# Optimization experiments

Hardware: AMD Instinct MI355X
Metric: run time of the kernel (lower is better)

Reference implementation:

```python
import jax, jax.numpy as jnp
import numpy as np

NUM_NODES = 100000
HIDDEN = 128
NUM_PATH = 8
PATH_LEN = 8


def setup_inputs() -> dict:
    key = jax.random.key(0)
    k1, k2, k3, k4, k5 = jax.random.split(key, 5)
    feats = jax.random.normal(k1, (NUM_NODES, HIDDEN), dtype=jnp.float32)
    paths = jax.random.randint(k2, (NUM_PATH, NUM_NODES, PATH_LEN), 0, NUM_NODES, dtype=jnp.int32)
    init_feats = jax.random.normal(k3, (NUM_NODES, HIDDEN), dtype=jnp.float32)
    # xavier_normal_ with gain=1.414 on (1, L, D): std = gain*sqrt(2/(fan_in+fan_out))
    pw_std = 1.414 * np.sqrt(2.0 / (PATH_LEN + HIDDEN))
    path_weight = pw_std * jax.random.normal(k4, (1, PATH_LEN, HIDDEN), dtype=jnp.float32)
    fc_std = 1.414 * np.sqrt(2.0 / (HIDDEN + HIDDEN))
    fc_w = fc_std * jax.random.normal(k5, (HIDDEN, HIDDEN), dtype=jnp.float32)
    return {"feats": feats, "paths": paths, "init_feats": init_feats,
            "path_weight": path_weight, "fc_w": fc_w}


def reference(feats, paths, init_feats, path_weight, fc_w):
    # feats: (N, D); paths: (P, N, L); path_weight: (1, L, D); fc_w: (D, D)
    w = path_weight[0]  # (L, D)

    def step(acc, path):
        g = feats[path]                      # (N, L, D) irregular gather
        acc = acc + jnp.einsum('nld,ld->nd', g, w)
        return acc, None

    acc, _ = jax.lax.scan(step, jnp.zeros_like(feats), paths)
    res = acc / paths.shape[0]               # mean over paths, (N, D)
    out = jax.nn.relu(res @ fc_w.T)          # Linear (no bias) + ReLU
    return out
```

## Files before the change

kernel.cpp:

```cpp
#include <hip/hip_runtime.h>
#include <hip/hip_fp16.h>


#define N_NODES 100000
#define HIDDEN  128
#define NPATH   8
#define PLEN    8
#define NPB     8
#define KT      32

__global__ void PathGCNLayer_61306363183203_tohalf(
    const float4* __restrict__ feats4,
    uint2*        __restrict__ fh)
{
    const size_t i = (size_t)blockIdx.x * blockDim.x + threadIdx.x;
    if (i < (size_t)N_NODES * 32) {
        const float4 v = feats4[i];
        __half2 a = __floats2half2_rn(v.x, v.y);
        __half2 b = __floats2half2_rn(v.z, v.w);
        uint2 o;
        o.x = *reinterpret_cast<unsigned int*>(&a);
        o.y = *reinterpret_cast<unsigned int*>(&b);
        fh[i] = o;
    }
}

__global__ void PathGCNLayer_61306363183203_fused_h(
    const uint2*  __restrict__ feats_h,
    const int*    __restrict__ paths,
    const float4* __restrict__ pw4,
    const float4* __restrict__ fcw4,
    float*        __restrict__ out)
{
    __shared__ int    sidx[NPATH * NPB * PLEN];
    __shared__ float4 sres4[NPB][33];
    __shared__ float  fcwt[HIDDEN][KT + 1];

    const int tid  = threadIdx.x;
    const int n0   = blockIdx.x * NPB;
    const int node = tid >> 5;
    const int c    = tid & 31;

    {
        const int p = tid >> 5;
        const int i = tid & 31;
        const size_t base = (size_t)p * (N_NODES * PLEN) + (size_t)n0 * PLEN;
        sidx[p * 64 + i]      = paths[base + i];
        sidx[p * 64 + i + 32] = paths[base + i + 32];
    }
    __syncthreads();

    float ax = 0.0f, ay = 0.0f, az = 0.0f, aw = 0.0f;
    #pragma unroll
    for (int l = 0; l < PLEN; ++l) {
        float sx = 0.0f, sy = 0.0f, sz = 0.0f, sw = 0.0f;
        #pragma unroll
        for (int p = 0; p < NPATH; ++p) {
            const int idx = sidx[p * 64 + node * PLEN + l];
            const uint2 hv = feats_h[(size_t)idx * 32 + c];
            const __half2 h0 = *reinterpret_cast<const __half2*>(&hv.x);
            const __half2 h1 = *reinterpret_cast<const __half2*>(&hv.y);
            const float2 f0 = __half22float2(h0);
            const float2 f1 = __half22float2(h1);
            sx += f0.x; sy += f0.y; sz += f1.x; sw += f1.y;
        }
        const float4 w = pw4[l * 32 + c];
        ax = fmaf(sx, w.x, ax);
        ay = fmaf(sy, w.y, ay);
        az = fmaf(sz, w.z, az);
        aw = fmaf(sw, w.w, aw);
    }
    {
        float4 r;
        r.x = ax * 0.125f; r.y = ay * 0.125f;
        r.z = az * 0.125f; r.w = aw * 0.125f;
        sres4[node][c] = r;
    }

    float o0 = 0.0f, o1 = 0.0f, o2 = 0.0f, o3 = 0.0f;

    #pragma unroll
    for (int kt = 0; kt < HIDDEN / KT; ++kt) {
        __syncthreads();
        {
            const int j    = tid >> 1;
            const int half = tid & 1;
            const int gbase = j * 32 + kt * (KT / 4) + half * 4;
            const int lbase = half * 16;
            #pragma unroll
            for (int q = 0; q < 4; ++q) {
                const float4 v = fcw4[gbase + q];
                fcwt[j][lbase + q * 4 + 0] = v.x;
                fcwt[j][lbase + q * 4 + 1] = v.y;
                fcwt[j][lbase + q * 4 + 2] = v.z;
                fcwt[j][lbase + q * 4 + 3] = v.w;
            }
        }
        __syncthreads();

        #pragma unroll
        for (int kc = 0; kc < KT / 4; ++kc) {
            const float4 rv = sres4[node][kt * (KT / 4) + kc];
            const int k0 = kc * 4;
            o0 = fmaf(rv.x, fcwt[c      ][k0    ], o0);
            o1 = fmaf(rv.x, fcwt[c + 32 ][k0    ], o1);
            o2 = fmaf(rv.x, fcwt[c + 64 ][k0    ], o2);
            o3 = fmaf(rv.x, fcwt[c + 96 ][k0    ], o3);
            o0 = fmaf(rv.y, fcwt[c      ][k0 + 1], o0);
            o1 = fmaf(rv.y, fcwt[c + 32 ][k0 + 1], o1);
            o2 = fmaf(rv.y, fcwt[c + 64 ][k0 + 1], o2);
            o3 = fmaf(rv.y, fcwt[c + 96 ][k0 + 1], o3);
            o0 = fmaf(rv.z, fcwt[c      ][k0 + 2], o0);
            o1 = fmaf(rv.z, fcwt[c + 32 ][k0 + 2], o1);
            o2 = fmaf(rv.z, fcwt[c + 64 ][k0 + 2], o2);
            o3 = fmaf(rv.z, fcwt[c + 96 ][k0 + 2], o3);
            o0 = fmaf(rv.w, fcwt[c      ][k0 + 3], o0);
            o1 = fmaf(rv.w, fcwt[c + 32 ][k0 + 3], o1);
            o2 = fmaf(rv.w, fcwt[c + 64 ][k0 + 3], o2);
            o3 = fmaf(rv.w, fcwt[c + 96 ][k0 + 3], o3);
        }
    }

    {
        const size_t obase = (size_t)(n0 + node) * HIDDEN + c;
        out[obase]      = o0 > 0.0f ? o0 : 0.0f;
        out[obase + 32] = o1 > 0.0f ? o1 : 0.0f;
        out[obase + 64] = o2 > 0.0f ? o2 : 0.0f;
        out[obase + 96] = o3 > 0.0f ? o3 : 0.0f;
    }
}

__global__ void PathGCNLayer_61306363183203_fused(
    const float4* __restrict__ feats4,
    const int*    __restrict__ paths,
    const float4* __restrict__ pw4,
    const float4* __restrict__ fcw4,
    float*        __restrict__ out)
{
    __shared__ int    sidx[NPATH * NPB * PLEN];
    __shared__ float4 sres4[NPB][33];
    __shared__ float  fcwt[HIDDEN][KT + 1];

    const int tid  = threadIdx.x;
    const int n0   = blockIdx.x * NPB;
    const int node = tid >> 5;
    const int c    = tid & 31;

    {
        const int p = tid >> 5;
        const int i = tid & 31;
        const size_t base = (size_t)p * (N_NODES * PLEN) + (size_t)n0 * PLEN;
        sidx[p * 64 + i]      = paths[base + i];
        sidx[p * 64 + i + 32] = paths[base + i + 32];
    }
    __syncthreads();

    float ax = 0.0f, ay = 0.0f, az = 0.0f, aw = 0.0f;
    #pragma unroll
    for (int l = 0; l < PLEN; ++l) {
        float sx = 0.0f, sy = 0.0f, sz = 0.0f, sw = 0.0f;
        #pragma unroll
        for (int p = 0; p < NPATH; ++p) {
            const int idx = sidx[p * 64 + node * PLEN + l];
            const float4 v = feats4[(size_t)idx * 32 + c];
            sx += v.x; sy += v.y; sz += v.z; sw += v.w;
        }
        const float4 w = pw4[l * 32 + c];
        ax = fmaf(sx, w.x, ax);
        ay = fmaf(sy, w.y, ay);
        az = fmaf(sz, w.z, az);
        aw = fmaf(sw, w.w, aw);
    }
    {
        float4 r;
        r.x = ax * 0.125f; r.y = ay * 0.125f;
        r.z = az * 0.125f; r.w = aw * 0.125f;
        sres4[node][c] = r;
    }

    float o0 = 0.0f, o1 = 0.0f, o2 = 0.0f, o3 = 0.0f;
    #pragma unroll
    for (int kt = 0; kt < HIDDEN / KT; ++kt) {
        __syncthreads();
        {
            const int j    = tid >> 1;
            const int half = tid & 1;
            const int gbase = j * 32 + kt * (KT / 4) + half * 4;
            const int lbase = half * 16;
            #pragma unroll
            for (int q = 0; q < 4; ++q) {
                const float4 v = fcw4[gbase + q];
                fcwt[j][lbase + q * 4 + 0] = v.x;
                fcwt[j][lbase + q * 4 + 1] = v.y;
                fcwt[j][lbase + q * 4 + 2] = v.z;
                fcwt[j][lbase + q * 4 + 3] = v.w;
            }
        }
        __syncthreads();
        #pragma unroll
        for (int kc = 0; kc < KT / 4; ++kc) {
            const float4 rv = sres4[node][kt * (KT / 4) + kc];
            const int k0 = kc * 4;
            o0 = fmaf(rv.x, fcwt[c      ][k0    ], o0);
            o1 = fmaf(rv.x, fcwt[c + 32 ][k0    ], o1);
            o2 = fmaf(rv.x, fcwt[c + 64 ][k0    ], o2);
            o3 = fmaf(rv.x, fcwt[c + 96 ][k0    ], o3);
            o0 = fmaf(rv.y, fcwt[c      ][k0 + 1], o0);
            o1 = fmaf(rv.y, fcwt[c + 32 ][k0 + 1], o1);
            o2 = fmaf(rv.y, fcwt[c + 64 ][k0 + 1], o2);
            o3 = fmaf(rv.y, fcwt[c + 96 ][k0 + 1], o3);
            o0 = fmaf(rv.z, fcwt[c      ][k0 + 2], o0);
            o1 = fmaf(rv.z, fcwt[c + 32 ][k0 + 2], o1);
            o2 = fmaf(rv.z, fcwt[c + 64 ][k0 + 2], o2);
            o3 = fmaf(rv.z, fcwt[c + 96 ][k0 + 2], o3);
            o0 = fmaf(rv.w, fcwt[c      ][k0 + 3], o0);
            o1 = fmaf(rv.w, fcwt[c + 32 ][k0 + 3], o1);
            o2 = fmaf(rv.w, fcwt[c + 64 ][k0 + 3], o2);
            o3 = fmaf(rv.w, fcwt[c + 96 ][k0 + 3], o3);
        }
    }
    {
        const size_t obase = (size_t)(n0 + node) * HIDDEN + c;
        out[obase]      = o0 > 0.0f ? o0 : 0.0f;
        out[obase + 32] = o1 > 0.0f ? o1 : 0.0f;
        out[obase + 64] = o2 > 0.0f ? o2 : 0.0f;
        out[obase + 96] = o3 > 0.0f ? o3 : 0.0f;
    }
}

extern "C" void kernel_launch(void* const* d_in, const int* in_sizes, int n_in,
                              void* d_out, int out_size, void* d_ws, size_t ws_size,
                              hipStream_t stream) {
    const float4* feats4 = (const float4*)d_in[0];
    const int*    paths  = (const int*)d_in[1];
    const float4* pw4    = (const float4*)d_in[3];
    const float4* fcw4   = (const float4*)d_in[4];
    float* out = (float*)d_out;
    (void)in_sizes; (void)n_in; (void)out_size;

    const size_t half_bytes = (size_t)N_NODES * HIDDEN * sizeof(unsigned short);
    if (d_ws != nullptr && ws_size >= half_bytes) {
        uint2* fh = (uint2*)d_ws;
        const int cvt_blocks = (N_NODES * 32 + 255) / 256;
        PathGCNLayer_61306363183203_tohalf<<<cvt_blocks, 256, 0, stream>>>(feats4, fh);
        PathGCNLayer_61306363183203_fused_h<<<N_NODES / NPB, 256, 0, stream>>>(
            fh, paths, pw4, fcw4, out);
    } else {
        PathGCNLayer_61306363183203_fused<<<N_NODES / NPB, 256, 0, stream>>>(
            feats4, paths, pw4, fcw4, out);
    }
}
```

Before: 367.5 us.

## Process 16 nodes per block with 16-byte half gathers and 8 outputs per thread

The half-precision fused kernel now handles 16 nodes per 256-thread block, with 16 threads per node. Each thread gathers a uint4 (8 halves) per neighbour instead of a uint2, and all 8 path loads are issued before accumulating. Each thread also computes 8 output columns in the FC stage, so the transposed weight tile is loaded once for twice as many nodes. The aim is wider memory transactions, more loads in flight and less redundant weight staging, at the cost of higher register use per thread.

```diff
diff --git a/kernel.cpp b/kernel.cpp
--- a/kernel.cpp
+++ b/kernel.cpp
@@ -6,7 +6,7 @@
 #define HIDDEN  128
 #define NPATH   8
 #define PLEN    8
-#define NPB     8
+#define NPB     16
 #define KT      32
 
 __global__ void PathGCNLayer_61306363183203_tohalf(
@@ -25,8 +25,8 @@
     }
 }
 
-__global__ void PathGCNLayer_61306363183203_fused_h(
-    const uint2*  __restrict__ feats_h,
+__global__ void PathGCNLayer_61306363183203_fused_h16(
+    const uint4*  __restrict__ feats_h4,
     const int*    __restrict__ paths,
     const float4* __restrict__ pw4,
     const float4* __restrict__ fcw4,
@@ -38,46 +38,78 @@
 
     const int tid  = threadIdx.x;
     const int n0   = blockIdx.x * NPB;
-    const int node = tid >> 5;
-    const int c    = tid & 31;
+    const int node = tid >> 4;
+    const int c    = tid & 15;
 
     {
         const int p = tid >> 5;
         const int i = tid & 31;
         const size_t base = (size_t)p * (N_NODES * PLEN) + (size_t)n0 * PLEN;
-        sidx[p * 64 + i]      = paths[base + i];
-        sidx[p * 64 + i + 32] = paths[base + i + 32];
+        sidx[p * 128 + i]      = paths[base + i];
+        sidx[p * 128 + i + 32] = paths[base + i + 32];
+        sidx[p * 128 + i + 64] = paths[base + i + 64];
+        sidx[p * 128 + i + 96] = paths[base + i + 96];
     }
     __syncthreads();
 
-    float ax = 0.0f, ay = 0.0f, az = 0.0f, aw = 0.0f;
+    float a0 = 0.f, a1 = 0.f, a2 = 0.f, a3 = 0.f,
+          a4 = 0.f, a5 = 0.f, a6 = 0.f, a7 = 0.f;
     #pragma unroll
     for (int l = 0; l < PLEN; ++l) {
-        float sx = 0.0f, sy = 0.0f, sz = 0.0f, sw = 0.0f;
-        #pragma unroll
-        for (int p = 0; p < NPATH; ++p) {
-            const int idx = sidx[p * 64 + node * PLEN + l];
-            const uint2 hv = feats_h[(size_t)idx * 32 + c];
-            const __half2 h0 = *reinterpret_cast<const __half2*>(&hv.x);
-            const __half2 h1 = *reinterpret_cast<const __half2*>(&hv.y);
-            const float2 f0 = __half22float2(h0);
-            const float2 f1 = __half22float2(h1);
-            sx += f0.x; sy += f0.y; sz += f1.x; sw += f1.y;
-        }
-        const float4 w = pw4[l * 32 + c];
-        ax = fmaf(sx, w.x, ax);
-        ay = fmaf(sy, w.y, ay);
-        az = fmaf(sz, w.z, az);
-        aw = fmaf(sw, w.w, aw);
-    }
-    {
-        float4 r;
-        r.x = ax * 0.125f; r.y = ay * 0.125f;
-        r.z = az * 0.125f; r.w = aw * 0.125f;
-        sres4[node][c] = r;
-    }
-
-    float o0 = 0.0f, o1 = 0.0f, o2 = 0.0f, o3 = 0.0f;
+        uint4 hv0, hv1, hv2, hv3, hv4, hv5, hv6, hv7;
+        {
+            const int i0 = sidx[0 * 128 + node * PLEN + l];
+            const int i1 = sidx[1 * 128 + node * PLEN + l];
+            const int i2 = sidx[2 * 128 + node * PLEN + l];
+            const int i3 = sidx[3 * 128 + node * PLEN + l];
+            const int i4 = sidx[4 * 128 + node * PLEN + l];
+            const int i5 = sidx[5 * 128 + node * PLEN + l];
+            const int i6 = sidx[6 * 128 + node * PLEN + l];
+            const int i7 = sidx[7 * 128 + node * PLEN + l];
+            hv0 = feats_h4[(size_t)i0 * 16 + c];
+            hv1 = feats_h4[(size_t)i1 * 16 + c];
+            hv2 = feats_h4[(size_t)i2 * 16 + c];
+            hv3 = feats_h4[(size_t)i3 * 16 + c];
+            hv4 = feats_h4[(size_t)i4 * 16 + c];
+            hv5 = feats_h4[(size_t)i5 * 16 + c];
+            hv6 = feats_h4[(size_t)i6 * 16 + c];
+            hv7 = feats_h4[(size_t)i7 * 16 + c];
+        }
+        float s0 = 0.f, s1 = 0.f, s2 = 0.f, s3 = 0.f,
+              s4 = 0.f, s5 = 0.f, s6 = 0.f, s7 = 0.f;
+        #define ACC8(hv)                                                            \
+        {                                                                           \
+            const float2 f0 = __half22float2(*reinterpret_cast<const __half2*>(&hv.x)); \
+            const float2 f1 = __half22float2(*reinterpret_cast<const __half2*>(&hv.y)); \
+            const float2 f2 = __half22float2(*reinterpret_cast<const __half2*>(&hv.z)); \
+            const float2 f3 = __half22float2(*reinterpret_cast<const __half2*>(&hv.w)); \
+            s0 += f0.x; s1 += f0.y; s2 += f1.x; s3 += f1.y;                         \
+            s4 += f2.x; s5 += f2.y; s6 += f3.x; s7 += f3.y;                         \
+        }
+        ACC8(hv0) ACC8(hv1) ACC8(hv2) ACC8(hv3)
+        ACC8(hv4) ACC8(hv5) ACC8(hv6) ACC8(hv7)
+        #undef ACC8
+        const float4 w0 = pw4[l * 32 + 2 * c];
+        const float4 w1 = pw4[l * 32 + 2 * c + 1];
+        a0 = fmaf(s0, w0.x, a0);
+        a1 = fmaf(s1, w0.y, a1);
+        a2 = fmaf(s2, w0.z, a2);
+        a3 = fmaf(s3, w0.w, a3);
+        a4 = fmaf(s4, w1.x, a4);
+        a5 = fmaf(s5, w1.y, a5);
+        a6 = fmaf(s6, w1.z, a6);
+        a7 = fmaf(s7, w1.w, a7);
+    }
+    {
+        float4 r0, r1;
+        r0.x = a0 * 0.125f; r0.y = a1 * 0.125f; r0.z = a2 * 0.125f; r0.w = a3 * 0.125f;
+        r1.x = a4 * 0.125f; r1.y = a5 * 0.125f; r1.z = a6 * 0.125f; r1.w = a7 * 0.125f;
+        sres4[node][2 * c]     = r0;
+        sres4[node][2 * c + 1] = r1;
+    }
+
+    float o0 = 0.f, o1 = 0.f, o2 = 0.f, o3 = 0.f,
+          o4 = 0.f, o5 = 0.f, o6 = 0.f, o7 = 0.f;
 
     #pragma unroll
     for (int kt = 0; kt < HIDDEN / KT; ++kt) {
@@ -98,6 +130,106 @@
         }
         __syncthreads();
 
+        #pragma unroll
+        for (int kc = 0; kc < KT / 4; ++kc) {
+            const float4 rv = sres4[node][kt * (KT / 4) + kc];
+            const int k0 = kc * 4;
+            #pragma unroll
+            for (int jj = 0; jj < 8; ++jj) {
+                const int j = c + 16 * jj;
+                float* op = (jj == 0) ? &o0 : (jj == 1) ? &o1 : (jj == 2) ? &o2 :
+                            (jj == 3) ? &o3 : (jj == 4) ? &o4 : (jj == 5) ? &o5 :
+                            (jj == 6) ? &o6 : &o7;
+                float o = *op;
+                o = fmaf(rv.x, fcwt[j][k0    ], o);
+                o = fmaf(rv.y, fcwt[j][k0 + 1], o);
+                o = fmaf(rv.z, fcwt[j][k0 + 2], o);
+                o = fmaf(rv.w, fcwt[j][k0 + 3], o);
+                *op = o;
+            }
+        }
+    }
+
+    {
+        const size_t obase = (size_t)(n0 + node) * HIDDEN + c;
+        out[obase      ] = o0 > 0.f ? o0 : 0.f;
+        out[obase + 16 ] = o1 > 0.f ? o1 : 0.f;
+        out[obase + 32 ] = o2 > 0.f ? o2 : 0.f;
+        out[obase + 48 ] = o3 > 0.f ? o3 : 0.f;
+        out[obase + 64 ] = o4 > 0.f ? o4 : 0.f;
+        out[obase + 80 ] = o5 > 0.f ? o5 : 0.f;
+        out[obase + 96 ] = o6 > 0.f ? o6 : 0.f;
+        out[obase + 112] = o7 > 0.f ? o7 : 0.f;
+    }
+}
+
+__global__ void PathGCNLayer_61306363183203_fused(
+    const float4* __restrict__ feats4,
+    const int*    __restrict__ paths,
+    const float4* __restrict__ pw4,
+    const float4* __restrict__ fcw4,
+    float*        __restrict__ out)
+{
+    __shared__ int    sidx[NPATH * 8 * PLEN];
+    __shared__ float4 sres4[8][33];
+    __shared__ float  fcwt[HIDDEN][KT + 1];
+
+    const int tid  = threadIdx.x;
+    const int n0   = blockIdx.x * 8;
+    const int node = tid >> 5;
+    const int c    = tid & 31;
+
+    {
+        const int p = tid >> 5;
+        const int i = tid & 31;
+        const size_t base = (size_t)p * (N_NODES * PLEN) + (size_t)n0 * PLEN;
+        sidx[p * 64 + i]      = paths[base + i];
+        sidx[p * 64 + i + 32] = paths[base + i + 32];
+    }
+    __syncthreads();
+
+    float ax = 0.0f, ay = 0.0f, az = 0.0f, aw = 0.0f;
+    #pragma unroll
+    for (int l = 0; l < PLEN; ++l) {
+        float sx = 0.0f, sy = 0.0f, sz = 0.0f, sw = 0.0f;
+        #pragma unroll
+        for (int p = 0; p < NPATH; ++p) {
+            const int idx = sidx[p * 64 + node * PLEN + l];
+            const float4 v = feats4[(size_t)idx * 32 + c];
+            sx += v.x; sy += v.y; sz += v.z; sw += v.w;
+        }
+        const float4 w = pw4[l * 32 + c];
+        ax = fmaf(sx, w.x, ax);
+        ay = fmaf(sy, w.y, ay);
+        az = fmaf(sz, w.z, az);
+        aw = fmaf(sw, w.w, aw);
+    }
+    {
+        float4 r;
+        r.x = ax * 0.125f; r.y = ay * 0.125f;
+        r.z = az * 0.125f; r.w = aw * 0.125f;
+        sres4[node][c] = r;
+    }
+
+    float o0 = 0.0f, o1 = 0.0f, o2 = 0.0f, o3 = 0.0f;
+    #pragma unroll
+    for (int kt = 0; kt < HIDDEN / KT; ++kt) {
+        __syncthreads();
+        {
+            const int j    = tid >> 1;
+            const int half = tid & 1;
+            const int gbase = j * 32 + kt * (KT / 4) + half * 4;
+            const int lbase = half * 16;
+            #pragma unroll
+            for (int q = 0; q < 4; ++q) {
+                const float4 v = fcw4[gbase + q];
+                fcwt[j][lbase + q * 4 + 0] = v.x;
+                fcwt[j][lbase + q * 4 + 1] = v.y;
+                fcwt[j][lbase + q * 4 + 2] = v.z;
+                fcwt[j][lbase + q * 4 + 3] = v.w;
+            }
+        }
+        __syncthreads();
         #pragma unroll
         for (int kc = 0; kc < KT / 4; ++kc) {
             const float4 rv = sres4[node][kt * (KT / 4) + kc];
@@ -120,105 +252,6 @@
             o3 = fmaf(rv.w, fcwt[c + 96 ][k0 + 3], o3);
         }
     }
-
-    {
-        const size_t obase = (size_t)(n0 + node) * HIDDEN + c;
-        out[obase]      = o0 > 0.0f ? o0 : 0.0f;
-        out[obase + 32] = o1 > 0.0f ? o1 : 0.0f;
-        out[obase + 64] = o2 > 0.0f ? o2 : 0.0f;
-        out[obase + 96] = o3 > 0.0f ? o3 : 0.0f;
-    }
-}
-
-__global__ void PathGCNLayer_61306363183203_fused(
-    const float4* __restrict__ feats4,
-    const int*    __restrict__ paths,
-    const float4* __restrict__ pw4,
-    const float4* __restrict__ fcw4,
-    float*        __restrict__ out)
-{
-    __shared__ int    sidx[NPATH * NPB * PLEN];
-    __shared__ float4 sres4[NPB][33];
-    __shared__ float  fcwt[HIDDEN][KT + 1];
-
-    const int tid  = threadIdx.x;
-    const int n0   = blockIdx.x * NPB;
-    const int node = tid >> 5;
-    const int c    = tid & 31;
-
-    {
-        const int p = tid >> 5;
-        const int i = tid & 31;
-        const size_t base = (size_t)p * (N_NODES * PLEN) + (size_t)n0 * PLEN;
-        sidx[p * 64 + i]      = paths[base + i];
-        sidx[p * 64 + i + 32] = paths[base + i + 32];
-    }
-    __syncthreads();
-
-    float ax = 0.0f, ay = 0.0f, az = 0.0f, aw = 0.0f;
-    #pragma unroll
-    for (int l = 0; l < PLEN; ++l) {
-        float sx = 0.0f, sy = 0.0f, sz = 0.0f, sw = 0.0f;
-        #pragma unroll
-        for (int p = 0; p < NPATH; ++p) {
-            const int idx = sidx[p * 64 + node * PLEN + l];
-            const float4 v = feats4[(size_t)idx * 32 + c];
-            sx += v.x; sy += v.y; sz += v.z; sw += v.w;
-        }
-        const float4 w = pw4[l * 32 + c];
-        ax = fmaf(sx, w.x, ax);
-        ay = fmaf(sy, w.y, ay);
-        az = fmaf(sz, w.z, az);
-        aw = fmaf(sw, w.w, aw);
-    }
-    {
-        float4 r;
-        r.x = ax * 0.125f; r.y = ay * 0.125f;
-        r.z = az * 0.125f; r.w = aw * 0.125f;
-        sres4[node][c] = r;
-    }
-
-    float o0 = 0.0f, o1 = 0.0f, o2 = 0.0f, o3 = 0.0f;
-    #pragma unroll
-    for (int kt = 0; kt < HIDDEN / KT; ++kt) {
-        __syncthreads();
-        {
-            const int j    = tid >> 1;
-            const int half = tid & 1;
-            const int gbase = j * 32 + kt * (KT / 4) + half * 4;
-            const int lbase = half * 16;
-            #pragma unroll
-            for (int q = 0; q < 4; ++q) {
-                const float4 v = fcw4[gbase + q];
-                fcwt[j][lbase + q * 4 + 0] = v.x;
-                fcwt[j][lbase + q * 4 + 1] = v.y;
-                fcwt[j][lbase + q * 4 + 2] = v.z;
-                fcwt[j][lbase + q * 4 + 3] = v.w;
-            }
-        }
-        __syncthreads();
-        #pragma unroll
-        for (int kc = 0; kc < KT / 4; ++kc) {
-            const float4 rv = sres4[node][kt * (KT / 4) + kc];
-            const int k0 = kc * 4;
-            o0 = fmaf(rv.x, fcwt[c      ][k0    ], o0);
-            o1 = fmaf(rv.x, fcwt[c + 32 ][k0    ], o1);
-            o2 = fmaf(rv.x, fcwt[c + 64 ][k0    ], o2);
-            o3 = fmaf(rv.x, fcwt[c + 96 ][k0    ], o3);
-            o0 = fmaf(rv.y, fcwt[c      ][k0 + 1], o0);
-            o1 = fmaf(rv.y, fcwt[c + 32 ][k0 + 1], o1);
-            o2 = fmaf(rv.y, fcwt[c + 64 ][k0 + 1], o2);
-            o3 = fmaf(rv.y, fcwt[c + 96 ][k0 + 1], o3);
-            o0 = fmaf(rv.z, fcwt[c      ][k0 + 2], o0);
-            o1 = fmaf(rv.z, fcwt[c + 32 ][k0 + 2], o1);
-            o2 = fmaf(rv.z, fcwt[c + 64 ][k0 + 2], o2);
-            o3 = fmaf(rv.z, fcwt[c + 96 ][k0 + 2], o3);
-            o0 = fmaf(rv.w, fcwt[c      ][k0 + 3], o0);
-            o1 = fmaf(rv.w, fcwt[c + 32 ][k0 + 3], o1);
-            o2 = fmaf(rv.w, fcwt[c + 64 ][k0 + 3], o2);
-            o3 = fmaf(rv.w, fcwt[c + 96 ][k0 + 3], o3);
-        }
-    }
     {
         const size_t obase = (size_t)(n0 + node) * HIDDEN + c;
         out[obase]      = o0 > 0.0f ? o0 : 0.0f;
@@ -243,10 +276,10 @@
         uint2* fh = (uint2*)d_ws;
         const int cvt_blocks = (N_NODES * 32 + 255) / 256;
         PathGCNLayer_61306363183203_tohalf<<<cvt_blocks, 256, 0, stream>>>(feats4, fh);
-        PathGCNLayer_61306363183203_fused_h<<<N_NODES / NPB, 256, 0, stream>>>(
-            fh, paths, pw4, fcw4, out);
+        PathGCNLayer_61306363183203_fused_h16<<<N_NODES / NPB, 256, 0, stream>>>(
+            (const uint4*)d_ws, paths, pw4, fcw4, out);
     } else {
-        PathGCNLayer_61306363183203_fused<<<N_NODES / NPB, 256, 0, stream>>>(
+        PathGCNLayer_61306363183203_fused<<<N_NODES / 8, 256, 0, stream>>>(
             feats4, paths, pw4, fcw4, out);
     }
 }
```

Measured after the change: 450.9 us. +22.7%, slower.
